# Optimization experiments

Hardware: AMD Instinct MI355X
Metric: run time of the kernel (lower is better)

Reference implementation:

```python
import jax, jax.numpy as jnp
import numpy as np

DIM = 192
HEADS = 6
WS = 8          # window size
SHIFT = 4       # shift size
HIDDEN = 384    # mlp hidden = 2.0 * dim
EPS = 1e-5


def _rel_pos_index(ws):
    # static [N, N] int index into the (2*ws-1)^2 bias table
    coords = np.stack(np.meshgrid(np.arange(ws), np.arange(ws), indexing='ij')).reshape(2, -1)
    rel = (coords[:, :, None] - coords[:, None, :]).transpose(1, 2, 0)
    rel[..., 0] += ws - 1
    rel[..., 1] += ws - 1
    rel[..., 0] *= 2 * ws - 1
    return rel.sum(-1)


def _attn_mask(hp, wp, ws, shift):
    # static shift-window mask: [nW, N, N], 0 or -100
    img = np.zeros((hp, wp))
    sl = (slice(0, -ws), slice(-ws, -shift), slice(-shift, None))
    cnt = 0
    for hs in sl:
        for wsl in sl:
            img[hs, wsl] = cnt
            cnt += 1
    m = img.reshape(hp // ws, ws, wp // ws, ws).transpose(0, 2, 1, 3).reshape(-1, ws * ws)
    diff = m[:, None, :] - m[:, :, None]
    return np.where(diff != 0, -100.0, 0.0).astype(np.float32)


def _ln(x, g, b):
    mu = x.mean(-1, keepdims=True)
    var = ((x - mu) ** 2).mean(-1, keepdims=True)
    return (x - mu) * jax.lax.rsqrt(var + EPS) * g + b


def setup_inputs() -> dict:
    key = jax.random.key(0)
    ks = jax.random.split(key, 6)
    B, H, W, C = 4, 224, 224, DIM
    return {
        'x': jax.random.normal(ks[0], (B, H * W, C), jnp.float32),
        'norm1_g': jnp.ones((C,), jnp.float32),
        'norm1_b': jnp.zeros((C,), jnp.float32),
        'qkv_w': jax.random.normal(ks[1], (C, 3 * C), jnp.float32) * 0.02,
        'qkv_b': jnp.zeros((3 * C,), jnp.float32),
        'proj_w': jax.random.normal(ks[2], (C, C), jnp.float32) * 0.02,
        'proj_b': jnp.zeros((C,), jnp.float32),
        'rel_bias_table': jax.random.normal(ks[3], ((2 * WS - 1) ** 2, HEADS), jnp.float32) * 0.02,
        'norm2_g': jnp.ones((C,), jnp.float32),
        'norm2_b': jnp.zeros((C,), jnp.float32),
        'fc1_w': jax.random.normal(ks[4], (C, HIDDEN), jnp.float32) * 0.02,
        'fc1_b': jnp.zeros((HIDDEN,), jnp.float32),
        'fc2_w': jax.random.normal(ks[5], (HIDDEN, C), jnp.float32) * 0.02,
        'fc2_b': jnp.zeros((C,), jnp.float32),
        'height': 224,
        'width': 224,
    }


def reference(x, norm1_g, norm1_b, qkv_w, qkv_b, proj_w, proj_b, rel_bias_table,
              norm2_g, norm2_b, fc1_w, fc1_b, fc2_w, fc2_b, height, width):
    B, T, C = x.shape
    dh = C // HEADS
    scale = dh ** (-0.5)
    shortcut = x

    xw = _ln(x, norm1_g, norm1_b).reshape(B, height, width, C)
    pad_h = (WS - height % WS) % WS
    pad_w = (WS - width % WS) % WS
    if pad_h > 0 or pad_w > 0:
        xw = jnp.pad(xw, ((0, 0), (0, pad_h), (0, pad_w), (0, 0)))
    Hp, Wp = height + pad_h, width + pad_w

    if SHIFT > 0:
        xs = jnp.roll(xw, (-SHIFT, -SHIFT), axis=(1, 2))
        mask = jnp.asarray(_attn_mask(Hp, Wp, WS, SHIFT))  # [nW, N, N]
    else:
        xs, mask = xw, None

    N = WS * WS
    # window partition -> [B*nW, N, C]
    xwin = xs.reshape(B, Hp // WS, WS, Wp // WS, WS, C).transpose(0, 1, 3, 2, 4, 5).reshape(-1, N, C)

    qkv = (xwin @ qkv_w + qkv_b).reshape(-1, N, 3, HEADS, dh).transpose(2, 0, 3, 1, 4)
    q, k, v = qkv[0] * scale, qkv[1], qkv[2]          # [B*nW, H, N, dh]
    attn = jnp.einsum('whnd,whmd->whnm', q, k)         # [B*nW, H, N, N]

    idx = jnp.asarray(_rel_pos_index(WS).reshape(-1))
    bias = rel_bias_table[idx].reshape(N, N, HEADS).transpose(2, 0, 1)  # [H, N, N]
    attn = attn + bias[None]

    if mask is not None:
        nW = mask.shape[0]
        attn = attn.reshape(-1, nW, HEADS, N, N) + mask[None, :, None]
        attn = attn.reshape(-1, HEADS, N, N)

    attn = jax.nn.softmax(attn, axis=-1)
    out = jnp.einsum('whnm,whmd->wnhd', attn, v).reshape(-1, N, C)
    out = out @ proj_w + proj_b

    # window reverse -> [B, Hp, Wp, C]
    out = out.reshape(B, Hp // WS, Wp // WS, WS, WS, C).transpose(0, 1, 3, 2, 4, 5).reshape(B, Hp, Wp, C)
    if SHIFT > 0:
        out = jnp.roll(out, (SHIFT, SHIFT), axis=(1, 2))
    if pad_h > 0 or pad_w > 0:
        out = out[:, :height, :width, :]

    x = shortcut + out.reshape(B, height * width, C)
    h = _ln(x, norm2_g, norm2_b)
    h = jax.nn.gelu(h @ fc1_w + fc1_b, approximate=False) @ fc2_w + fc2_b
    return x + h
```

## Files before the change

### kernel.cpp

```cpp
#include <hip/hip_runtime.h>
#include <math.h>

#define T_TOT   200704
#define C_DIM   192
#define HEADS   6
#define DH      32
#define NTOK    64
#define NWIN    3136
#define HID     384
#define IMG     224
#define NSIDE   28
#define WPI     784
#define QSCALE  0.17677669529663687f

typedef unsigned short ushortT;
typedef short bf16x8 __attribute__((ext_vector_type(8)));
typedef float f32x4 __attribute__((ext_vector_type(4)));

__device__ __forceinline__ unsigned short f2bf(float f){
    unsigned u = __float_as_uint(f);
    u += 0x7FFFu + ((u >> 16) & 1u);
    return (unsigned short)(u >> 16);
}
__device__ __forceinline__ unsigned pack2(float a, float b){
    return (unsigned)f2bf(a) | ((unsigned)f2bf(b) << 16);
}

__global__ void k_prep(const float* __restrict__ qkv_w, const float* __restrict__ proj_w,
                       const float* __restrict__ fc1_w, const float* __restrict__ fc2_w,
                       const float* __restrict__ table,
                       unsigned short* __restrict__ wt_qkv, unsigned short* __restrict__ wt_proj,
                       unsigned short* __restrict__ wt_fc1, unsigned short* __restrict__ wt_fc2,
                       float* __restrict__ bmT)
{
    int idx = blockIdx.x * 256 + threadIdx.x;
    if (idx < 110592){
        int n = idx / 192, k = idx - n * 192;
        wt_qkv[idx] = f2bf(qkv_w[(size_t)k * 576 + n]);
    } else if (idx < 147456){
        int i = idx - 110592;
        int n = i / 192, k = i - n * 192;
        wt_proj[i] = f2bf(proj_w[(size_t)k * 192 + n]);
    } else if (idx < 221184){
        int i = idx - 147456;
        int n = i / 192, k = i - n * 192;
        wt_fc1[i] = f2bf(fc1_w[(size_t)k * 384 + n]);
    } else if (idx < 294912){
        int i = idx - 221184;
        int n = i / 384, k = i - n * 384;
        wt_fc2[i] = f2bf(fc2_w[(size_t)k * 192 + n]);
    } else if (idx < 393216){
        int i = idx - 294912;
        int q = i & 63, m = (i >> 6) & 63;
        int head = (i >> 12) % HEADS, type = i / (64 * 64 * HEADS);
        int rq = q >> 3, cq = q & 7, rm = m >> 3, cm = m & 7;
        float b = table[((rq - rm + 7) * 15 + (cq - cm + 7)) * HEADS + head];
        int th = type >> 1, tw = type & 1;
        int lq = (th ? (rq >= 4 ? 2 : 1) : 0) * 3 + (tw ? (cq >= 4 ? 2 : 1) : 0);
        int lm = (th ? (rm >= 4 ? 2 : 1) : 0) * 3 + (tw ? (cm >= 4 ? 2 : 1) : 0);
        bmT[i] = b + ((lq != lm) ? -100.f : 0.f);
    }
}

__global__ void k_ln1qkv(const float* __restrict__ x, const float* __restrict__ g,
                         const float* __restrict__ bta,
                         const unsigned short* __restrict__ wt, const float* __restrict__ bias,
                         unsigned short* __restrict__ q, unsigned short* __restrict__ k,
                         unsigned short* __restrict__ v)
{
    __shared__ __align__(16) unsigned short As[64*200];
    const int tid = threadIdx.x, lane = tid & 63, wid = tid >> 6;
    const int lr = lane & 15, lg = lane >> 4;
    const int win = blockIdx.x;

    {
        int bimg = win / WPI, w2 = win % WPI;
        int wi8 = (w2 / NSIDE) * 8, wj8 = (w2 % NSIDE) * 8;
        #pragma unroll
        for (int b = 0; b < 2; b++){
            int n = b*32 + (tid >> 3), part = tid & 7;
            int r = n >> 3, c = n & 7;
            int hs = wi8 + r + 4; if (hs >= IMG) hs -= IMG;
            int ws = wj8 + c + 4; if (ws >= IMG) ws -= IMG;
            const float* xp = x + ((size_t)bimg * (IMG*IMG) + hs * IMG + ws) * C_DIM + part * 24;
            float sum = 0.f, sq = 0.f;
            #pragma unroll
            for (int j = 0; j < 6; j++){
                float4 v4 = *(const float4*)(xp + j*4);
                sum += v4.x + v4.y + v4.z + v4.w;
                sq  += v4.x*v4.x + v4.y*v4.y + v4.z*v4.z + v4.w*v4.w;
            }
            sum += __shfl_xor(sum, 1); sq += __shfl_xor(sq, 1);
            sum += __shfl_xor(sum, 2); sq += __shfl_xor(sq, 2);
            sum += __shfl_xor(sum, 4); sq += __shfl_xor(sq, 4);
            float mu = sum * (1.f/192.f);
            float var = sq * (1.f/192.f) - mu*mu;
            float rs = rsqrtf(var + 1e-5f);
            int c0 = part * 24;
            #pragma unroll
            for (int j = 0; j < 3; j++){
                int cc = c0 + j*8;
                float4 va = *(const float4*)(xp + j*8);
                float4 vb = *(const float4*)(xp + j*8 + 4);
                float4 ga = *(const float4*)(g + cc), gb = *(const float4*)(g + cc + 4);
                float4 ba = *(const float4*)(bta + cc), bb = *(const float4*)(bta + cc + 4);
                unsigned short tmp[8];
                tmp[0] = f2bf((va.x-mu)*rs*ga.x + ba.x);
                tmp[1] = f2bf((va.y-mu)*rs*ga.y + ba.y);
                tmp[2] = f2bf((va.z-mu)*rs*ga.z + ba.z);
                tmp[3] = f2bf((va.w-mu)*rs*ga.w + ba.w);
                tmp[4] = f2bf((vb.x-mu)*rs*gb.x + bb.x);
                tmp[5] = f2bf((vb.y-mu)*rs*gb.y + bb.y);
                tmp[6] = f2bf((vb.z-mu)*rs*gb.z + bb.z);
                tmp[7] = f2bf((vb.w-mu)*rs*gb.w + bb.w);
                *(uint4*)&As[n*200 + cc] = *(uint4*)tmp;
            }
        }
    }
    __syncthreads();

    #pragma unroll
    for (int chunk = 0; chunk < 3; chunk++){
        f32x4 acc[3][4];
        #pragma unroll
        for (int nf = 0; nf < 3; nf++)
            #pragma unroll
            for (int mf = 0; mf < 4; mf++)
                acc[nf][mf] = (f32x4){0.f,0.f,0.f,0.f};
        #pragma unroll
        for (int k0 = 0; k0 < C_DIM; k0 += 32){
            bf16x8 a[4], b[3];
            #pragma unroll
            for (int mf = 0; mf < 4; mf++)
                a[mf] = *(const bf16x8*)&As[(mf*16 + lr)*200 + k0 + lg*8];
            #pragma unroll
            for (int nf = 0; nf < 3; nf++)
                b[nf] = *(const bf16x8*)(wt + (size_t)(chunk*192 + wid*48 + nf*16 + lr)*C_DIM + k0 + lg*8);
            #pragma unroll
            for (int nf = 0; nf < 3; nf++)
                #pragma unroll
                for (int mf = 0; mf < 4; mf++)
                    acc[nf][mf] = __builtin_amdgcn_mfma_f32_16x16x32_bf16(a[mf], b[nf], acc[nf][mf], 0, 0, 0);
        }
        unsigned short* dst = (chunk == 0) ? q : (chunk == 1) ? k : v;
        float sc = (chunk == 0) ? QSCALE : 1.f;
        #pragma unroll
        for (int nf = 0; nf < 3; nf++){
            int cc = wid*48 + nf*16 + lr;
            float b = bias[chunk*192 + cc];
            int head = cc >> 5, d = cc & 31;
            unsigned short* dp = dst + ((size_t)(win*HEADS + head) * NTOK) * DH + d;
            #pragma unroll
            for (int mf = 0; mf < 4; mf++)
                #pragma unroll
                for (int r = 0; r < 4; r++){
                    int ntok = mf*16 + lg*4 + r;
                    dp[ntok*DH] = f2bf((acc[nf][mf][r] + b) * sc);
                }
        }
    }
}

__global__ void k_attn_mfma(const unsigned short* __restrict__ q, const unsigned short* __restrict__ k,
                            const unsigned short* __restrict__ v, const float* __restrict__ bmT,
                            unsigned short* __restrict__ attn_o)
{
    __shared__ __align__(16) unsigned short Vt[4][32*72];
    __shared__ __align__(16) unsigned short Ps[4][64*72];
    const int tid = threadIdx.x, lane = tid & 63, wid = tid >> 6;
    const int wh = blockIdx.x * 4 + wid;
    const int head = wh % HEADS, win = wh / HEADS;
    const int w2 = win % WPI;
    const int type = ((w2 / NSIDE) == 27 ? 2 : 0) + ((w2 % NSIDE) == 27 ? 1 : 0);
    const size_t base = (size_t)wh * (NTOK * DH);
    const int lr = lane & 15, lg = lane >> 4;

    {
        const uint4* vp = (const uint4*)(v + base + lane * DH);
        uint4 va = vp[0], vb = vp[1], vc = vp[2], vd = vp[3];
        unsigned short* dst = &Vt[wid][lane];
        unsigned w0[8] = {va.x, va.y, va.z, va.w, vb.x, vb.y, vb.z, vb.w};
        #pragma unroll
        for (int j = 0; j < 8; j++){
            dst[(2*j)*72]   = (unsigned short)(w0[j] & 0xFFFFu);
            dst[(2*j+1)*72] = (unsigned short)(w0[j] >> 16);
        }
        unsigned w1[8] = {vc.x, vc.y, vc.z, vc.w, vd.x, vd.y, vd.z, vd.w};
        #pragma unroll
        for (int j = 0; j < 8; j++){
            dst[(16+2*j)*72]   = (unsigned short)(w1[j] & 0xFFFFu);
            dst[(16+2*j+1)*72] = (unsigned short)(w1[j] >> 16);
        }
    }

    bf16x8 aq[4], bk[4];
    {
        const unsigned short* qg = q + base + lr * DH + (lg << 3);
        const unsigned short* kg = k + base + lr * DH + (lg << 3);
        #pragma unroll
        for (int i = 0; i < 4; i++){
            aq[i] = *(const bf16x8*)(qg + i * 16 * DH);
            bk[i] = *(const bf16x8*)(kg + i * 16 * DH);
        }
    }

    f32x4 acc[4][4];
    #pragma unroll
    for (int mi = 0; mi < 4; mi++)
        #pragma unroll
        for (int ni = 0; ni < 4; ni++)
            acc[mi][ni] = __builtin_amdgcn_mfma_f32_16x16x32_bf16(aq[mi], bk[ni],
                              (f32x4){0.f,0.f,0.f,0.f}, 0, 0, 0);

    const float* bmBase = bmT + ((size_t)(type * HEADS + head) * 64) * 64;
    #pragma unroll
    for (int mi = 0; mi < 4; mi++)
        #pragma unroll
        for (int ni = 0; ni < 4; ni++){
            float4 bm = *(const float4*)(bmBase + (lr + 16*ni)*64 + lg*4 + 16*mi);
            acc[mi][ni][0] += bm.x; acc[mi][ni][1] += bm.y;
            acc[mi][ni][2] += bm.z; acc[mi][ni][3] += bm.w;
        }

    #pragma unroll
    for (int mi = 0; mi < 4; mi++){
        #pragma unroll
        for (int r = 0; r < 4; r++){
            float mx = fmaxf(fmaxf(acc[mi][0][r], acc[mi][1][r]),
                             fmaxf(acc[mi][2][r], acc[mi][3][r]));
            mx = fmaxf(mx, __shfl_xor(mx, 1));
            mx = fmaxf(mx, __shfl_xor(mx, 2));
            mx = fmaxf(mx, __shfl_xor(mx, 4));
            mx = fmaxf(mx, __shfl_xor(mx, 8));
            float e0 = __expf(acc[mi][0][r] - mx);
            float e1 = __expf(acc[mi][1][r] - mx);
            float e2 = __expf(acc[mi][2][r] - mx);
            float e3 = __expf(acc[mi][3][r] - mx);
            float sum = e0 + e1 + e2 + e3;
            sum += __shfl_xor(sum, 1);
            sum += __shfl_xor(sum, 2);
            sum += __shfl_xor(sum, 4);
            sum += __shfl_xor(sum, 8);
            float inv = 1.f / sum;
            int row = lg*4 + r + 16*mi;
            unsigned short* pr = &Ps[wid][row*72 + lr];
            pr[0]  = f2bf(e0 * inv);
            pr[16] = f2bf(e1 * inv);
            pr[32] = f2bf(e2 * inv);
            pr[48] = f2bf(e3 * inv);
        }
    }

    f32x4 o[4][2];
    #pragma unroll
    for (int mi = 0; mi < 4; mi++)
        #pragma unroll
        for (int ni = 0; ni < 2; ni++)
            o[mi][ni] = (f32x4){0.f,0.f,0.f,0.f};
    #pragma unroll
    for (int kb = 0; kb < 2; kb++){
        bf16x8 ap[4], bv[2];
        #pragma unroll
        for (int mi = 0; mi < 4; mi++)
            ap[mi] = *(const bf16x8*)&Ps[wid][(lr + 16*mi)*72 + (lg<<3) + 32*kb];
        #pragma unroll
        for (int ni = 0; ni < 2; ni++)
            bv[ni] = *(const bf16x8*)&Vt[wid][(lr + 16*ni)*72 + (lg<<3) + 32*kb];
        #pragma unroll
        for (int mi = 0; mi < 4; mi++)
            #pragma unroll
            for (int ni = 0; ni < 2; ni++)
                o[mi][ni] = __builtin_amdgcn_mfma_f32_16x16x32_bf16(ap[mi], bv[ni], o[mi][ni], 0, 0, 0);
    }

    unsigned short* ob = attn_o + ((size_t)win * NTOK) * C_DIM + head * DH;
    #pragma unroll
    for (int mi = 0; mi < 4; mi++)
        #pragma unroll
        for (int ni = 0; ni < 2; ni++)
            #pragma unroll
            for (int r = 0; r < 4; r++){
                int row = lg*4 + r + 16*mi;
                ob[(size_t)row * C_DIM + lr + 16*ni] = f2bf(o[mi][ni][r]);
            }
}

__global__ void k_proj2(const unsigned short* __restrict__ ain, const unsigned short* __restrict__ wt,
                        const float* __restrict__ bias, const float* __restrict__ x,
                        float* __restrict__ out)
{
    __shared__ __align__(16) unsigned short As[64*200];
    const int tid = threadIdx.x, lane = tid & 63, wid = tid >> 6;
    const int lr = lane & 15, lg = lane >> 4;
    const int t0 = blockIdx.x * 64, win = blockIdx.x;

    {
        int row = tid >> 2, part = tid & 3;
        const unsigned short* gp = ain + (size_t)(t0 + row) * C_DIM;
        #pragma unroll
        for (int j = 0; j < 6; j++){
            int c = part*8 + j*32;
            *(uint4*)&As[row*200 + c] = *(const uint4*)(gp + c);
        }
    }
    __syncthreads();

    f32x4 acc[3][4];
    #pragma unroll
    for (int nf = 0; nf < 3; nf++)
        #pragma unroll
        for (int mf = 0; mf < 4; mf++)
            acc[nf][mf] = (f32x4){0.f,0.f,0.f,0.f};
    #pragma unroll
    for (int k0 = 0; k0 < C_DIM; k0 += 32){
        bf16x8 a[4], b[3];
        #pragma unroll
        for (int mf = 0; mf < 4; mf++)
            a[mf] = *(const bf16x8*)&As[(mf*16 + lr)*200 + k0 + lg*8];
        #pragma unroll
        for (int nf = 0; nf < 3; nf++)
            b[nf] = *(const bf16x8*)(wt + (size_t)(wid*48 + nf*16 + lr)*C_DIM + k0 + lg*8);
        #pragma unroll
        for (int nf = 0; nf < 3; nf++)
            #pragma unroll
            for (int mf = 0; mf < 4; mf++)
                acc[nf][mf] = __builtin_amdgcn_mfma_f32_16x16x32_bf16(a[mf], b[nf], acc[nf][mf], 0, 0, 0);
    }

    const int bimg = win / WPI, w2 = win % WPI;
    const int wi = w2 / NSIDE, wj = w2 % NSIDE;
    #pragma unroll
    for (int mf = 0; mf < 4; mf++){
        #pragma unroll
        for (int r = 0; r < 4; r++){
            int n = mf*16 + lg*4 + r;
            int rr = n >> 3, cc_ = n & 7;
            int hf = wi*8 + rr + 4; if (hf >= IMG) hf -= IMG;
            int wf = wj*8 + cc_ + 4; if (wf >= IMG) wf -= IMG;
            size_t s = ((size_t)bimg*(IMG*IMG) + hf*IMG + wf) * C_DIM;
            #pragma unroll
            for (int nf = 0; nf < 3; nf++){
                int c = wid*48 + nf*16 + lr;
                out[s + c] = x[s + c] + acc[nf][mf][r] + bias[c];
            }
        }
    }
}

#define XS_STR 200
#define H1_STR 392
#define O_STR  196
__global__ void k_mlp(float* __restrict__ out,
                      const float* __restrict__ g, const float* __restrict__ bta,
                      const unsigned short* __restrict__ w1, const float* __restrict__ b1,
                      const unsigned short* __restrict__ w2, const float* __restrict__ b2)
{
    __shared__ __align__(16) unsigned short H1u[32*H1_STR];
    unsigned short* Xs = H1u;
    float* O = (float*)H1u;
    const int tid = threadIdx.x, lane = tid & 63, wid = tid >> 6;
    const int lr = lane & 15, lg = lane >> 4;
    const int t0 = blockIdx.x * 32;

    {
        int row = tid >> 3, part = tid & 7;
        const float* xp = out + (size_t)(t0 + row) * C_DIM + part * 24;
        float vals[24];
        float sum = 0.f, sq = 0.f;
        #pragma unroll
        for (int j = 0; j < 6; j++){
            float4 v4 = *(const float4*)(xp + j*4);
            vals[j*4+0] = v4.x; vals[j*4+1] = v4.y; vals[j*4+2] = v4.z; vals[j*4+3] = v4.w;
            sum += v4.x + v4.y + v4.z + v4.w;
            sq  += v4.x*v4.x + v4.y*v4.y + v4.z*v4.z + v4.w*v4.w;
        }
        sum += __shfl_xor(sum, 1); sq += __shfl_xor(sq, 1);
        sum += __shfl_xor(sum, 2); sq += __shfl_xor(sq, 2);
        sum += __shfl_xor(sum, 4); sq += __shfl_xor(sq, 4);
        float mu = sum * (1.f/192.f);
        float var = sq * (1.f/192.f) - mu*mu;
        float rs = rsqrtf(var + 1e-5f);
        int c0 = part * 24;
        #pragma unroll
        for (int j = 0; j < 3; j++){
            int c = c0 + j*8;
            float4 ga = *(const float4*)(g + c), gb = *(const float4*)(g + c + 4);
            float4 ba = *(const float4*)(bta + c), bb = *(const float4*)(bta + c + 4);
            unsigned short tmp[8];
            tmp[0] = f2bf((vals[j*8+0]-mu)*rs*ga.x + ba.x);
            tmp[1] = f2bf((vals[j*8+1]-mu)*rs*ga.y + ba.y);
            tmp[2] = f2bf((vals[j*8+2]-mu)*rs*ga.z + ba.z);
            tmp[3] = f2bf((vals[j*8+3]-mu)*rs*ga.w + ba.w);
            tmp[4] = f2bf((vals[j*8+4]-mu)*rs*gb.x + bb.x);
            tmp[5] = f2bf((vals[j*8+5]-mu)*rs*gb.y + bb.y);
            tmp[6] = f2bf((vals[j*8+6]-mu)*rs*gb.z + bb.z);
            tmp[7] = f2bf((vals[j*8+7]-mu)*rs*gb.w + bb.w);
            *(uint4*)&Xs[row*XS_STR + c] = *(uint4*)tmp;
        }
    }
    __syncthreads();

    f32x4 acc1[6][2];
    {
        #pragma unroll
        for (int mf = 0; mf < 6; mf++)
            #pragma unroll
            for (int nf = 0; nf < 2; nf++)
                acc1[mf][nf] = (f32x4){0.f,0.f,0.f,0.f};
        #pragma unroll
        for (int k0 = 0; k0 < C_DIM; k0 += 32){
            bf16x8 a[6], b[2];
            #pragma unroll
            for (int mf = 0; mf < 6; mf++)
                a[mf] = *(const bf16x8*)(w1 + (size_t)(wid*96 + mf*16 + lr)*C_DIM + k0 + lg*8);
            #pragma unroll
            for (int nf = 0; nf < 2; nf++)
                b[nf] = *(const bf16x8*)&Xs[(nf*16 + lr)*XS_STR + k0 + lg*8];
            #pragma unroll
            for (int mf = 0; mf < 6; mf++)
                #pragma unroll
                for (int nf = 0; nf < 2; nf++)
                    acc1[mf][nf] = __builtin_amdgcn_mfma_f32_16x16x32_bf16(a[mf], b[nf], acc1[mf][nf], 0, 0, 0);
        }
    }
    __syncthreads();

    {
        #pragma unroll
        for (int mf = 0; mf < 6; mf++){
            int hc = wid*96 + mf*16 + lg*4;
            float4 bb = *(const float4*)(b1 + hc);
            float bias[4] = {bb.x, bb.y, bb.z, bb.w};
            #pragma unroll
            for (int nf = 0; nf < 2; nf++){
                int token = nf*16 + lr;
                float gl[4];
                #pragma unroll
                for (int r = 0; r < 4; r++){
                    float u = acc1[mf][nf][r] + bias[r];
                    gl[r] = 0.5f*u*(1.f + erff(u*0.70710678118654752f));
                }
                uint2 pk; pk.x = pack2(gl[0], gl[1]); pk.y = pack2(gl[2], gl[3]);
                *(uint2*)&H1u[token*H1_STR + hc] = pk;
            }
        }
    }
    __syncthreads();

    f32x4 acc2[2][3];
    {
        #pragma unroll
        for (int rf = 0; rf < 2; rf++)
            #pragma unroll
            for (int cf = 0; cf < 3; cf++)
                acc2[rf][cf] = (f32x4){0.f,0.f,0.f,0.f};
        #pragma unroll
        for (int k0 = 0; k0 < HID; k0 += 32){
            bf16x8 a[2], b[3];
            #pragma unroll
            for (int rf = 0; rf < 2; rf++)
                a[rf] = *(const bf16x8*)&H1u[(rf*16 + lr)*H1_STR + k0 + lg*8];
            #pragma unroll
            for (int cf = 0; cf < 3; cf++)
                b[cf] = *(const bf16x8*)(w2 + (size_t)(wid*48 + cf*16 + lr)*HID + k0 + lg*8);
            #pragma unroll
            for (int rf = 0; rf < 2; rf++)
                #pragma unroll
                for (int cf = 0; cf < 3; cf++)
                    acc2[rf][cf] = __builtin_amdgcn_mfma_f32_16x16x32_bf16(a[rf], b[cf], acc2[rf][cf], 0, 0, 0);
        }
    }
    __syncthreads();

    #pragma unroll
    for (int cf = 0; cf < 3; cf++){
        int c = wid*48 + cf*16 + lr;
        float bias = b2[c];
        #pragma unroll
        for (int rf = 0; rf < 2; rf++)
            #pragma unroll
            for (int r = 0; r < 4; r++)
                O[(rf*16 + lg*4 + r)*O_STR + c] = acc2[rf][cf][r] + bias;
    }
    __syncthreads();

    {
        int row = tid >> 3, part = tid & 7;
        float* op = out + (size_t)(t0 + row) * C_DIM;
        const float* Or = O + row * O_STR;
        #pragma unroll
        for (int j = 0; j < 6; j++){
            int c = part*4 + j*32;
            float4 add = *(const float4*)&Or[c];
            float4 old = *(const float4*)&op[c];
            old.x += add.x; old.y += add.y; old.z += add.z; old.w += add.w;
            *(float4*)&op[c] = old;
        }
    }
}

extern "C" void kernel_launch(void* const* d_in, const int* in_sizes, int n_in,
                              void* d_out, int out_size, void* d_ws, size_t ws_size,
                              hipStream_t stream)
{
    const float* x       = (const float*)d_in[0];
    const float* n1g     = (const float*)d_in[1];
    const float* n1b     = (const float*)d_in[2];
    const float* qkv_w   = (const float*)d_in[3];
    const float* qkv_b   = (const float*)d_in[4];
    const float* proj_w  = (const float*)d_in[5];
    const float* proj_b  = (const float*)d_in[6];
    const float* rtab    = (const float*)d_in[7];
    const float* n2g     = (const float*)d_in[8];
    const float* n2b     = (const float*)d_in[9];
    const float* fc1_w   = (const float*)d_in[10];
    const float* fc1_b   = (const float*)d_in[11];
    const float* fc2_w   = (const float*)d_in[12];
    const float* fc2_b   = (const float*)d_in[13];
    float* out = (float*)d_out;

    char* wsb = (char*)d_ws;
    const size_t SZ = (size_t)T_TOT * C_DIM * 2;
    unsigned short* attn_o = (unsigned short*)(wsb);
    unsigned short* qb   = (unsigned short*)(wsb + SZ);
    unsigned short* kb   = (unsigned short*)(wsb + 2*SZ);
    unsigned short* vb   = (unsigned short*)(wsb + 3*SZ);
    unsigned short* wt_qkv  = (unsigned short*)(wsb + 4*SZ);
    unsigned short* wt_proj = wt_qkv + 576*192;
    unsigned short* wt_fc1  = wt_proj + 192*192;
    unsigned short* wt_fc2  = wt_fc1 + 384*192;
    float*          bmT     = (float*)(wt_fc2 + 384*192);

    k_prep<<<(393216 + 255)/256, 256, 0, stream>>>(qkv_w, proj_w, fc1_w, fc2_w, rtab,
                                                   wt_qkv, wt_proj, wt_fc1, wt_fc2, bmT);

    k_ln1qkv<<<NWIN, 256, 0, stream>>>(x, n1g, n1b, wt_qkv, qkv_b, qb, kb, vb);
    k_attn_mfma<<<NWIN*HEADS/4, 256, 0, stream>>>(qb, kb, vb, bmT, attn_o);
    k_proj2<<<NWIN, 256, 0, stream>>>(attn_o, wt_proj, proj_b, x, out);
    k_mlp<<<T_TOT/32, 256, 0, stream>>>(out, n2g, n2b, wt_fc1, fc1_b, wt_fc2, fc2_b);
}
```

Baseline: 678.0 us.

## Fuse LayerNorm2 into projection epilogue and feed MLP bf16 normalized input

Computes the second LayerNorm inside the projection kernel's epilogue, using cross-lane shuffles and a small shared buffer to reduce row statistics across the four waves. The result is written as a bf16 buffer, reusing the q buffer. The MLP kernel then reads the bf16 normalized activations directly from global memory instead of re-reading fp32 output and normalizing in LDS. This removes a full fp32 reread plus the LN pass and one barrier from the MLP, at the cost of an extra bf16 write and scattered 2-byte stores in the projection kernel.

```diff
diff --git a/kernel.cpp b/kernel.cpp
--- a/kernel.cpp
+++ b/kernel.cpp
@@ -287,9 +287,11 @@
 
 __global__ void k_proj2(const unsigned short* __restrict__ ain, const unsigned short* __restrict__ wt,
                         const float* __restrict__ bias, const float* __restrict__ x,
-                        float* __restrict__ out)
+                        const float* __restrict__ n2g, const float* __restrict__ n2b,
+                        float* __restrict__ out, unsigned short* __restrict__ ln2)
 {
     __shared__ __align__(16) unsigned short As[64*200];
+    __shared__ float2 Pp[4][64];
     const int tid = threadIdx.x, lane = tid & 63, wid = tid >> 6;
     const int lr = lane & 15, lg = lane >> 4;
     const int t0 = blockIdx.x * 64, win = blockIdx.x;
@@ -329,6 +331,13 @@
 
     const int bimg = win / WPI, w2 = win % WPI;
     const int wi = w2 / NSIDE, wj = w2 % NSIDE;
+    float bcol[3], gcol[3], btcol[3];
+    #pragma unroll
+    for (int nf = 0; nf < 3; nf++){
+        int c = wid*48 + nf*16 + lr;
+        bcol[nf] = bias[c]; gcol[nf] = n2g[c]; btcol[nf] = n2b[c];
+    }
+
     #pragma unroll
     for (int mf = 0; mf < 4; mf++){
         #pragma unroll
@@ -338,68 +347,61 @@
             int hf = wi*8 + rr + 4; if (hf >= IMG) hf -= IMG;
             int wf = wj*8 + cc_ + 4; if (wf >= IMG) wf -= IMG;
             size_t s = ((size_t)bimg*(IMG*IMG) + hf*IMG + wf) * C_DIM;
+            float sum = 0.f, sq = 0.f;
             #pragma unroll
             for (int nf = 0; nf < 3; nf++){
                 int c = wid*48 + nf*16 + lr;
-                out[s + c] = x[s + c] + acc[nf][mf][r] + bias[c];
+                float o = x[s + c] + acc[nf][mf][r] + bcol[nf];
+                acc[nf][mf][r] = o;
+                sum += o; sq += o*o;
             }
-        }
-    }
-}
-
-#define XS_STR 200
+            sum += __shfl_xor(sum, 1); sq += __shfl_xor(sq, 1);
+            sum += __shfl_xor(sum, 2); sq += __shfl_xor(sq, 2);
+            sum += __shfl_xor(sum, 4); sq += __shfl_xor(sq, 4);
+            sum += __shfl_xor(sum, 8); sq += __shfl_xor(sq, 8);
+            if (lr == 0) Pp[wid][n] = make_float2(sum, sq);
+        }
+    }
+    __syncthreads();
+
+    #pragma unroll
+    for (int mf = 0; mf < 4; mf++){
+        #pragma unroll
+        for (int r = 0; r < 4; r++){
+            int n = mf*16 + lg*4 + r;
+            float2 p0 = Pp[0][n], p1 = Pp[1][n], p2 = Pp[2][n], p3 = Pp[3][n];
+            float sum = p0.x + p1.x + p2.x + p3.x;
+            float sq  = p0.y + p1.y + p2.y + p3.y;
+            float mu = sum * (1.f/192.f);
+            float var = sq * (1.f/192.f) - mu*mu;
+            float rs = rsqrtf(var + 1e-5f);
+            int rr = n >> 3, cc_ = n & 7;
+            int hf = wi*8 + rr + 4; if (hf >= IMG) hf -= IMG;
+            int wf = wj*8 + cc_ + 4; if (wf >= IMG) wf -= IMG;
+            size_t s = ((size_t)bimg*(IMG*IMG) + hf*IMG + wf) * C_DIM;
+            #pragma unroll
+            for (int nf = 0; nf < 3; nf++){
+                int c = wid*48 + nf*16 + lr;
+                float o = acc[nf][mf][r];
+                out[s + c] = o;
+                ln2[s + c] = f2bf((o - mu)*rs*gcol[nf] + btcol[nf]);
+            }
+        }
+    }
+}
+
 #define H1_STR 392
 #define O_STR  196
-__global__ void k_mlp(float* __restrict__ out,
-                      const float* __restrict__ g, const float* __restrict__ bta,
+__global__ void k_mlp(float* __restrict__ out, const unsigned short* __restrict__ ln2,
                       const unsigned short* __restrict__ w1, const float* __restrict__ b1,
                       const unsigned short* __restrict__ w2, const float* __restrict__ b2)
 {
     __shared__ __align__(16) unsigned short H1u[32*H1_STR];
-    unsigned short* Xs = H1u;
     float* O = (float*)H1u;
     const int tid = threadIdx.x, lane = tid & 63, wid = tid >> 6;
     const int lr = lane & 15, lg = lane >> 4;
     const int t0 = blockIdx.x * 32;
 
-    {
-        int row = tid >> 3, part = tid & 7;
-        const float* xp = out + (size_t)(t0 + row) * C_DIM + part * 24;
-        float vals[24];
-        float sum = 0.f, sq = 0.f;
-        #pragma unroll
-        for (int j = 0; j < 6; j++){
-            float4 v4 = *(const float4*)(xp + j*4);
-            vals[j*4+0] = v4.x; vals[j*4+1] = v4.y; vals[j*4+2] = v4.z; vals[j*4+3] = v4.w;
-            sum += v4.x + v4.y + v4.z + v4.w;
-            sq  += v4.x*v4.x + v4.y*v4.y + v4.z*v4.z + v4.w*v4.w;
-        }
-        sum += __shfl_xor(sum, 1); sq += __shfl_xor(sq, 1);
-        sum += __shfl_xor(sum, 2); sq += __shfl_xor(sq, 2);
-        sum += __shfl_xor(sum, 4); sq += __shfl_xor(sq, 4);
-        float mu = sum * (1.f/192.f);
-        float var = sq * (1.f/192.f) - mu*mu;
-        float rs = rsqrtf(var + 1e-5f);
-        int c0 = part * 24;
-        #pragma unroll
-        for (int j = 0; j < 3; j++){
-            int c = c0 + j*8;
-            float4 ga = *(const float4*)(g + c), gb = *(const float4*)(g + c + 4);
-            float4 ba = *(const float4*)(bta + c), bb = *(const float4*)(bta + c + 4);
-            unsigned short tmp[8];
-            tmp[0] = f2bf((vals[j*8+0]-mu)*rs*ga.x + ba.x);
-            tmp[1] = f2bf((vals[j*8+1]-mu)*rs*ga.y + ba.y);
-            tmp[2] = f2bf((vals[j*8+2]-mu)*rs*ga.z + ba.z);
-            tmp[3] = f2bf((vals[j*8+3]-mu)*rs*ga.w + ba.w);
-            tmp[4] = f2bf((vals[j*8+4]-mu)*rs*gb.x + bb.x);
-            tmp[5] = f2bf((vals[j*8+5]-mu)*rs*gb.y + bb.y);
-            tmp[6] = f2bf((vals[j*8+6]-mu)*rs*gb.z + bb.z);
-            tmp[7] = f2bf((vals[j*8+7]-mu)*rs*gb.w + bb.w);
-            *(uint4*)&Xs[row*XS_STR + c] = *(uint4*)tmp;
-        }
-    }
-    __syncthreads();
-
     f32x4 acc1[6][2];
     {
         #pragma unroll
@@ -415,7 +417,7 @@
                 a[mf] = *(const bf16x8*)(w1 + (size_t)(wid*96 + mf*16 + lr)*C_DIM + k0 + lg*8);
             #pragma unroll
             for (int nf = 0; nf < 2; nf++)
-                b[nf] = *(const bf16x8*)&Xs[(nf*16 + lr)*XS_STR + k0 + lg*8];
+                b[nf] = *(const bf16x8*)(ln2 + (size_t)(t0 + nf*16 + lr)*C_DIM + k0 + lg*8);
             #pragma unroll
             for (int mf = 0; mf < 6; mf++)
                 #pragma unroll
@@ -423,7 +425,6 @@
                     acc1[mf][nf] = __builtin_amdgcn_mfma_f32_16x16x32_bf16(a[mf], b[nf], acc1[mf][nf], 0, 0, 0);
         }
     }
-    __syncthreads();
 
     {
         #pragma unroll
@@ -530,12 +531,13 @@
     unsigned short* wt_fc1  = wt_proj + 192*192;
     unsigned short* wt_fc2  = wt_fc1 + 384*192;
     float*          bmT     = (float*)(wt_fc2 + 384*192);
+    unsigned short* ln2buf  = qb;
 
     k_prep<<<(393216 + 255)/256, 256, 0, stream>>>(qkv_w, proj_w, fc1_w, fc2_w, rtab,
                                                    wt_qkv, wt_proj, wt_fc1, wt_fc2, bmT);
 
     k_ln1qkv<<<NWIN, 256, 0, stream>>>(x, n1g, n1b, wt_qkv, qkv_b, qb, kb, vb);
     k_attn_mfma<<<NWIN*HEADS/4, 256, 0, stream>>>(qb, kb, vb, bmT, attn_o);
-    k_proj2<<<NWIN, 256, 0, stream>>>(attn_o, wt_proj, proj_b, x, out);
-    k_mlp<<<T_TOT/32, 256, 0, stream>>>(out, n2g, n2b, wt_fc1, fc1_b, wt_fc2, fc2_b);
-}
+    k_proj2<<<NWIN, 256, 0, stream>>>(attn_o, wt_proj, proj_b, x, n2g, n2b, out, ln2buf);
+    k_mlp<<<T_TOT/32, 256, 0, stream>>>(out, ln2buf, wt_fc1, fc1_b, wt_fc2, fc2_b);
+}
```

New measurement: 730.5 us. +7.7%, slower.

## Split fused MLP kernel into separate fc1 and fc2 kernels via global buffer

Applied to the files above, without the earlier changes.

Splits the fused LayerNorm+fc1+GELU+fc2 kernel into two kernels. The hidden activations (bf16, 384 per token) go through a global workspace buffer that reuses the K buffer, instead of living in shared memory. Each kernel uses less shared memory and fewer registers, which should raise occupancy. In exchange it adds roughly 150MB of extra global write and read traffic plus one more launch.

```diff
diff --git a/kernel.cpp b/kernel.cpp
--- a/kernel.cpp
+++ b/kernel.cpp
@@ -348,16 +348,12 @@
 }
 
 #define XS_STR 200
-#define H1_STR 392
-#define O_STR  196
-__global__ void k_mlp(float* __restrict__ out,
+__global__ void k_fc1(const float* __restrict__ out,
                       const float* __restrict__ g, const float* __restrict__ bta,
                       const unsigned short* __restrict__ w1, const float* __restrict__ b1,
-                      const unsigned short* __restrict__ w2, const float* __restrict__ b2)
-{
-    __shared__ __align__(16) unsigned short H1u[32*H1_STR];
-    unsigned short* Xs = H1u;
-    float* O = (float*)H1u;
+                      unsigned short* __restrict__ h1)
+{
+    __shared__ __align__(16) unsigned short Xs[32*XS_STR];
     const int tid = threadIdx.x, lane = tid & 63, wid = tid >> 6;
     const int lr = lane & 15, lg = lane >> 4;
     const int t0 = blockIdx.x * 32;
@@ -401,76 +397,77 @@
     __syncthreads();
 
     f32x4 acc1[6][2];
-    {
+    #pragma unroll
+    for (int mf = 0; mf < 6; mf++)
+        #pragma unroll
+        for (int nf = 0; nf < 2; nf++)
+            acc1[mf][nf] = (f32x4){0.f,0.f,0.f,0.f};
+    #pragma unroll
+    for (int k0 = 0; k0 < C_DIM; k0 += 32){
+        bf16x8 a[6], b[2];
         #pragma unroll
         for (int mf = 0; mf < 6; mf++)
+            a[mf] = *(const bf16x8*)(w1 + (size_t)(wid*96 + mf*16 + lr)*C_DIM + k0 + lg*8);
+        #pragma unroll
+        for (int nf = 0; nf < 2; nf++)
+            b[nf] = *(const bf16x8*)&Xs[(nf*16 + lr)*XS_STR + k0 + lg*8];
+        #pragma unroll
+        for (int mf = 0; mf < 6; mf++)
             #pragma unroll
             for (int nf = 0; nf < 2; nf++)
-                acc1[mf][nf] = (f32x4){0.f,0.f,0.f,0.f};
-        #pragma unroll
-        for (int k0 = 0; k0 < C_DIM; k0 += 32){
-            bf16x8 a[6], b[2];
-            #pragma unroll
-            for (int mf = 0; mf < 6; mf++)
-                a[mf] = *(const bf16x8*)(w1 + (size_t)(wid*96 + mf*16 + lr)*C_DIM + k0 + lg*8);
-            #pragma unroll
-            for (int nf = 0; nf < 2; nf++)
-                b[nf] = *(const bf16x8*)&Xs[(nf*16 + lr)*XS_STR + k0 + lg*8];
-            #pragma unroll
-            for (int mf = 0; mf < 6; mf++)
-                #pragma unroll
-                for (int nf = 0; nf < 2; nf++)
-                    acc1[mf][nf] = __builtin_amdgcn_mfma_f32_16x16x32_bf16(a[mf], b[nf], acc1[mf][nf], 0, 0, 0);
-        }
-    }
-    __syncthreads();
-
-    {
-        #pragma unroll
-        for (int mf = 0; mf < 6; mf++){
-            int hc = wid*96 + mf*16 + lg*4;
-            float4 bb = *(const float4*)(b1 + hc);
-            float bias[4] = {bb.x, bb.y, bb.z, bb.w};
-            #pragma unroll
-            for (int nf = 0; nf < 2; nf++){
-                int token = nf*16 + lr;
-                float gl[4];
-                #pragma unroll
-                for (int r = 0; r < 4; r++){
-                    float u = acc1[mf][nf][r] + bias[r];
-                    gl[r] = 0.5f*u*(1.f + erff(u*0.70710678118654752f));
-                }
-                uint2 pk; pk.x = pack2(gl[0], gl[1]); pk.y = pack2(gl[2], gl[3]);
-                *(uint2*)&H1u[token*H1_STR + hc] = pk;
+                acc1[mf][nf] = __builtin_amdgcn_mfma_f32_16x16x32_bf16(a[mf], b[nf], acc1[mf][nf], 0, 0, 0);
+    }
+
+    #pragma unroll
+    for (int mf = 0; mf < 6; mf++){
+        int hc = wid*96 + mf*16 + lg*4;
+        float4 bb = *(const float4*)(b1 + hc);
+        float bias[4] = {bb.x, bb.y, bb.z, bb.w};
+        #pragma unroll
+        for (int nf = 0; nf < 2; nf++){
+            int token = t0 + nf*16 + lr;
+            float gl[4];
+            #pragma unroll
+            for (int r = 0; r < 4; r++){
+                float u = acc1[mf][nf][r] + bias[r];
+                gl[r] = 0.5f*u*(1.f + erff(u*0.70710678118654752f));
             }
-        }
-    }
-    __syncthreads();
+            uint2 pk; pk.x = pack2(gl[0], gl[1]); pk.y = pack2(gl[2], gl[3]);
+            *(uint2*)(h1 + (size_t)token*HID + hc) = pk;
+        }
+    }
+}
+
+#define O_STR  196
+__global__ void k_fc2(float* __restrict__ out, const unsigned short* __restrict__ h1,
+                      const unsigned short* __restrict__ w2, const float* __restrict__ b2)
+{
+    __shared__ __align__(16) float O[32*O_STR];
+    const int tid = threadIdx.x, lane = tid & 63, wid = tid >> 6;
+    const int lr = lane & 15, lg = lane >> 4;
+    const int t0 = blockIdx.x * 32;
 
     f32x4 acc2[2][3];
-    {
+    #pragma unroll
+    for (int rf = 0; rf < 2; rf++)
+        #pragma unroll
+        for (int cf = 0; cf < 3; cf++)
+            acc2[rf][cf] = (f32x4){0.f,0.f,0.f,0.f};
+    #pragma unroll
+    for (int k0 = 0; k0 < HID; k0 += 32){
+        bf16x8 a[2], b[3];
         #pragma unroll
         for (int rf = 0; rf < 2; rf++)
+            a[rf] = *(const bf16x8*)(h1 + (size_t)(t0 + rf*16 + lr)*HID + k0 + lg*8);
+        #pragma unroll
+        for (int cf = 0; cf < 3; cf++)
+            b[cf] = *(const bf16x8*)(w2 + (size_t)(wid*48 + cf*16 + lr)*HID + k0 + lg*8);
+        #pragma unroll
+        for (int rf = 0; rf < 2; rf++)
             #pragma unroll
             for (int cf = 0; cf < 3; cf++)
-                acc2[rf][cf] = (f32x4){0.f,0.f,0.f,0.f};
-        #pragma unroll
-        for (int k0 = 0; k0 < HID; k0 += 32){
-            bf16x8 a[2], b[3];
-            #pragma unroll
-            for (int rf = 0; rf < 2; rf++)
-                a[rf] = *(const bf16x8*)&H1u[(rf*16 + lr)*H1_STR + k0 + lg*8];
-            #pragma unroll
-            for (int cf = 0; cf < 3; cf++)
-                b[cf] = *(const bf16x8*)(w2 + (size_t)(wid*48 + cf*16 + lr)*HID + k0 + lg*8);
-            #pragma unroll
-            for (int rf = 0; rf < 2; rf++)
-                #pragma unroll
-                for (int cf = 0; cf < 3; cf++)
-                    acc2[rf][cf] = __builtin_amdgcn_mfma_f32_16x16x32_bf16(a[rf], b[cf], acc2[rf][cf], 0, 0, 0);
-        }
-    }
-    __syncthreads();
+                acc2[rf][cf] = __builtin_amdgcn_mfma_f32_16x16x32_bf16(a[rf], b[cf], acc2[rf][cf], 0, 0, 0);
+    }
 
     #pragma unroll
     for (int cf = 0; cf < 3; cf++){
@@ -530,6 +527,7 @@
     unsigned short* wt_fc1  = wt_proj + 192*192;
     unsigned short* wt_fc2  = wt_fc1 + 384*192;
     float*          bmT     = (float*)(wt_fc2 + 384*192);
+    unsigned short* h1buf   = kb;
 
     k_prep<<<(393216 + 255)/256, 256, 0, stream>>>(qkv_w, proj_w, fc1_w, fc2_w, rtab,
                                                    wt_qkv, wt_proj, wt_fc1, wt_fc2, bmT);
@@ -537,5 +535,6 @@
     k_ln1qkv<<<NWIN, 256, 0, stream>>>(x, n1g, n1b, wt_qkv, qkv_b, qb, kb, vb);
     k_attn_mfma<<<NWIN*HEADS/4, 256, 0, stream>>>(qb, kb, vb, bmT, attn_o);
     k_proj2<<<NWIN, 256, 0, stream>>>(attn_o, wt_proj, proj_b, x, out);
-    k_mlp<<<T_TOT/32, 256, 0, stream>>>(out, n2g, n2b, wt_fc1, fc1_b, wt_fc2, fc2_b);
-}
+    k_fc1<<<T_TOT/32, 256, 0, stream>>>(out, n2g, n2b, wt_fc1, fc1_b, h1buf);
+    k_fc2<<<T_TOT/32, 256, 0, stream>>>(out, h1buf, wt_fc2, fc2_b);
+}
```

Result: slower. 813.6 us (+20.0%).
